# Performance work log

Measured on AMD Instinct MI355X. Metric: run time of the kernel, lower is better.

The kernel has to match this reference:

```python
import jax, jax.numpy as jnp
import numpy as np
import math

N = 20000      # nodes
E = 640000     # edges (avg degree 32)
G = 128        # g_dim (input features)
H1 = 128       # rgcn output dim
H2 = 128       # transformer output dim
R = 8          # num_relations


def setup_inputs() -> dict:
    key = jax.random.key(0)
    ks = jax.random.split(key, 12)
    x = jax.random.normal(ks[0], (N, G), dtype=jnp.float32)
    edge_index = jax.random.randint(ks[1], (2, E), 0, N)
    edge_type = jax.random.randint(ks[2], (E,), 0, R)
    s_in = 1.0 / math.sqrt(G)
    s_h1 = 1.0 / math.sqrt(H1)
    return {
        'x': x,
        'edge_index': edge_index,
        'edge_type': edge_type,
        # RGCNConv params (per-relation weights + root weight + bias)
        'rgcn_weight': jax.random.normal(ks[3], (R, G, H1), dtype=jnp.float32) * s_in,
        'rgcn_root': jax.random.normal(ks[4], (G, H1), dtype=jnp.float32) * s_in,
        'rgcn_bias': jnp.zeros((H1,), dtype=jnp.float32),
        # TransformerConv params (heads=1): query/key/value + skip linear
        'Wq': jax.random.normal(ks[5], (H1, H2), dtype=jnp.float32) * s_h1,
        'bq': jnp.zeros((H2,), dtype=jnp.float32),
        'Wk': jax.random.normal(ks[6], (H1, H2), dtype=jnp.float32) * s_h1,
        'bk': jnp.zeros((H2,), dtype=jnp.float32),
        'Wv': jax.random.normal(ks[7], (H1, H2), dtype=jnp.float32) * s_h1,
        'bv': jnp.zeros((H2,), dtype=jnp.float32),
        'Ws': jax.random.normal(ks[8], (H1, H2), dtype=jnp.float32) * s_h1,
        'bs': jnp.zeros((H2,), dtype=jnp.float32),
    }


def reference(x, edge_index, edge_type, rgcn_weight, rgcn_root, rgcn_bias,
              Wq, bq, Wk, bk, Wv, bv, Ws, bs):
    n = x.shape[0]
    src, dst = edge_index[0], edge_index[1]

    # ---- RGCNConv (aggr='mean' per relation, root weight + bias) ----
    # transform nodes by every relation, then gather per-edge message
    xr = jnp.einsum('ni,rio->nro', x, rgcn_weight)          # [N, R, H1]
    msg = xr[src, edge_type]                                # [E, H1]
    # per (dst, relation) edge counts for mean aggregation
    cnt = jnp.zeros((n, rgcn_weight.shape[0]), x.dtype).at[dst, edge_type].add(1.0)
    denom = jnp.maximum(cnt[dst, edge_type], 1.0)[:, None]  # [E, 1]
    agg = jnp.zeros((n, rgcn_weight.shape[2]), x.dtype).at[dst].add(msg / denom)
    h = agg + x @ rgcn_root + rgcn_bias
    h = jax.nn.relu(h)

    # ---- TransformerConv (heads=1, concat, root_weight=True) ----
    d = Wq.shape[1]
    q = h @ Wq + bq                                          # [N, H2]
    k = h @ Wk + bk
    v = h @ Wv + bv
    score = jnp.sum(q[dst] * k[src], axis=-1) / math.sqrt(d) # [E]
    # softmax over incoming edges of each destination node
    smax = jax.ops.segment_max(score, dst, num_segments=n)   # [N]
    e = jnp.exp(score - smax[dst])                           # [E]
    den = jax.ops.segment_sum(e, dst, num_segments=n)        # [N]
    alpha = e / jnp.maximum(den[dst], 1e-16)                 # [E]
    out = jax.ops.segment_sum(alpha[:, None] * v[src], dst, num_segments=n)
    out = out + h @ Ws + bs                                  # skip connection
    return jax.nn.relu(out)
```

## Files before the change

kernel.cpp:

```cpp
#include <hip/hip_runtime.h>

typedef unsigned short u16;
typedef unsigned int u32;
typedef __attribute__((ext_vector_type(8))) short short8;
typedef __attribute__((ext_vector_type(4))) float f32x4;

#define NN 20000
#define EE 640000
#define SCAN_BLOCKS 80

__device__ inline u16 f2bf(float f) {
    u32 x = __float_as_uint(f);
    return (u16)((x + 0x7FFFu + ((x >> 16) & 1u)) >> 16);
}
__device__ inline float lo16(u32 w) { return __uint_as_float(w << 16); }
__device__ inline float hi16(u32 w) { return __uint_as_float(w & 0xFFFF0000u); }
__device__ inline u32 packbf(float a, float b) { return ((u32)f2bf(b) << 16) | (u32)f2bf(a); }

#define ZP_N (NN * 8)
#define CX_N (NN * 32)
#define WP_N (128 * 1152 + 4 * 128 * 128 + 512)
__global__ __launch_bounds__(256) void prep_all(const float* __restrict__ x,
                                                const float* rw, const float* root,
                                                const float* Wq, const float* Wk,
                                                const float* Wv, const float* Ws,
                                                const float* bq, const float* bk,
                                                const float* bv, const float* bs,
                                                int* __restrict__ cnt, u16* __restrict__ xb,
                                                u16* wt1, u16* wt2, float* bcat) {
    int idx = blockIdx.x * 256 + threadIdx.x;
    if (idx < ZP_N) {
        cnt[idx] = 0;
        return;
    }
    idx -= ZP_N;
    if (idx < CX_N) {
        float4 v = *(const float4*)(x + (size_t)idx * 4);
        uint2 o;
        o.x = packbf(v.x, v.y);
        o.y = packbf(v.z, v.w);
        *(uint2*)(xb + (size_t)idx * 4) = o;
        return;
    }
    idx -= CX_N;
    const int S1 = 128 * 1152, S2 = 4 * 128 * 128;
    if (idx < S1) {
        int o = idx / 1152, k = idx - o * 1152;
        float v = (k < 1024) ? rw[k * 128 + o] : root[(k - 1024) * 128 + o];
        wt1[idx] = f2bf(v);
    } else if (idx < S1 + S2) {
        int j = idx - S1;
        int y = j >> 14, rem = j & 16383, o = rem >> 7, i = rem & 127;
        const float* W = (y == 0) ? Wq : (y == 1) ? Wk : (y == 2) ? Wv : Ws;
        wt2[j] = f2bf(W[i * 128 + o]);
    } else if (idx < S1 + S2 + 512) {
        int j = idx - (S1 + S2);
        int y = j >> 7, c = j & 127;
        const float* b = (y == 0) ? bq : (y == 1) ? bk : (y == 2) ? bv : bs;
        bcat[j] = b[c];
    }
}

__global__ void count_rank(const int* __restrict__ ei, const int* __restrict__ et,
                           int* __restrict__ cnt, int* __restrict__ rank) {
    int base = blockIdx.x * 2048 + threadIdx.x;
#pragma unroll
    for (int j = 0; j < 8; j++) {
        int e = base + j * 256;
        if (e < EE) {
            int dst = ei[EE + e];
            int r = et[e];
            rank[e] = atomicAdd(&cnt[dst * 8 + r], 1);
        }
    }
}

__global__ __launch_bounds__(256) void scan_phase1(const int* __restrict__ cnt,
                                                   int* __restrict__ deg_pref,
                                                   int* __restrict__ blk_sums) {
    __shared__ int lds[256];
    int t = threadIdx.x;
    int n = blockIdx.x * 256 + t;
    int d = 0;
    if (n < NN) {
        int4 c0 = *(const int4*)(cnt + n * 8);
        int4 c1 = *(const int4*)(cnt + n * 8 + 4);
        d = c0.x + c0.y + c0.z + c0.w + c1.x + c1.y + c1.z + c1.w;
    }
    lds[t] = d;
    __syncthreads();
    for (int o = 1; o < 256; o <<= 1) {
        int v = (t >= o) ? lds[t - o] : 0;
        __syncthreads();
        lds[t] += v;
        __syncthreads();
    }
    if (n < NN) deg_pref[n] = lds[t];
    if (t == 255) blk_sums[blockIdx.x] = lds[255];
}

__global__ __launch_bounds__(256) void scan_phase3(const int* __restrict__ cnt,
                                                   const int* __restrict__ deg_pref,
                                                   const int* __restrict__ blk_sums,
                                                   int* __restrict__ row_off,
                                                   int* __restrict__ srt) {
    __shared__ int bs_lds[128];
    int t = threadIdx.x;
    if (t < 128) {
        int v = (t < SCAN_BLOCKS) ? blk_sums[t] : 0;
        bs_lds[t] = v;
    }
    __syncthreads();
    if (t < 128) {
        for (int o = 1; o < 128; o <<= 1) {
            int a = (t >= o) ? bs_lds[t - o] : 0;
            __syncthreads();
            bs_lds[t] += a;
            __syncthreads();
        }
    } else {
        for (int o = 1; o < 128; o <<= 1) {
            __syncthreads();
            __syncthreads();
        }
    }
    int blk_excl = (blockIdx.x > 0) ? bs_lds[blockIdx.x - 1] : 0;
    int n = blockIdx.x * 256 + t;
    if (n >= NN) return;
    int4 c0 = *(const int4*)(cnt + n * 8);
    int4 c1 = *(const int4*)(cnt + n * 8 + 4);
    int deg = c0.x + c0.y + c0.z + c0.w + c1.x + c1.y + c1.z + c1.w;
    int start = blk_excl + deg_pref[n] - deg;
    row_off[n] = start;
    int sub = start;
    int o[8];
    o[0] = sub; sub += c0.x;
    o[1] = sub; sub += c0.y;
    o[2] = sub; sub += c0.z;
    o[3] = sub; sub += c0.w;
    o[4] = sub; sub += c1.x;
    o[5] = sub; sub += c1.y;
    o[6] = sub; sub += c1.z;
    o[7] = sub; sub += c1.w;
    *(int4*)(srt + n * 8) = make_int4(o[0], o[1], o[2], o[3]);
    *(int4*)(srt + n * 8 + 4) = make_int4(o[4], o[5], o[6], o[7]);
    if (n == NN - 1) row_off[NN] = sub;
}

__global__ void scatter_kernel(const int* __restrict__ ei, const int* __restrict__ et,
                               const int* __restrict__ srt, const int* __restrict__ rank,
                               int* __restrict__ es) {
    int base = blockIdx.x * 2048 + threadIdx.x;
#pragma unroll
    for (int j = 0; j < 8; j++) {
        int e = base + j * 256;
        if (e < EE) {
            int dst = ei[EE + e];
            int src = ei[e];
            int r = et[e];
            es[srt[dst * 8 + r] + rank[e]] = src;
        }
    }
}

__global__ __launch_bounds__(256) void rgcn_agg(const u16* __restrict__ xb,
                                                const int* __restrict__ srt,
                                                const int* __restrict__ cnt,
                                                const int* __restrict__ es,
                                                u16* __restrict__ pre) {
    int gid = blockIdx.x * 16 + (threadIdx.x >> 4);
    int lane = threadIdx.x & 15;
    if (gid >= NN * 9) return;
    int node = gid / 9;
    int slot = gid - node * 9;
    long prebase = (long)node * 1152;
    if (slot == 8) {
        uint4 xv = *(const uint4*)(xb + (long)node * 128 + lane * 8);
        *(uint4*)(pre + prebase + 1024 + lane * 8) = xv;
        return;
    }
    int c = cnt[node * 8 + slot];
    int p0 = srt[node * 8 + slot];
    float inv = 1.0f / (float)(c > 1 ? c : 1);
    float a0 = 0.f, a1 = 0.f, a2 = 0.f, a3 = 0.f, a4 = 0.f, a5 = 0.f, a6 = 0.f, a7 = 0.f;
    int i = 0;
    for (; i + 4 <= c; i += 4) {
        int s0 = es[p0 + i], s1 = es[p0 + i + 1], s2 = es[p0 + i + 2], s3 = es[p0 + i + 3];
        uint4 w0 = *(const uint4*)(xb + (long)s0 * 128 + lane * 8);
        uint4 w1 = *(const uint4*)(xb + (long)s1 * 128 + lane * 8);
        uint4 w2 = *(const uint4*)(xb + (long)s2 * 128 + lane * 8);
        uint4 w3 = *(const uint4*)(xb + (long)s3 * 128 + lane * 8);
        a0 += (lo16(w0.x) + lo16(w1.x)) + (lo16(w2.x) + lo16(w3.x));
        a1 += (hi16(w0.x) + hi16(w1.x)) + (hi16(w2.x) + hi16(w3.x));
        a2 += (lo16(w0.y) + lo16(w1.y)) + (lo16(w2.y) + lo16(w3.y));
        a3 += (hi16(w0.y) + hi16(w1.y)) + (hi16(w2.y) + hi16(w3.y));
        a4 += (lo16(w0.z) + lo16(w1.z)) + (lo16(w2.z) + lo16(w3.z));
        a5 += (hi16(w0.z) + hi16(w1.z)) + (hi16(w2.z) + hi16(w3.z));
        a6 += (lo16(w0.w) + lo16(w1.w)) + (lo16(w2.w) + lo16(w3.w));
        a7 += (hi16(w0.w) + hi16(w1.w)) + (hi16(w2.w) + hi16(w3.w));
    }
    for (; i < c; i++) {
        int s = es[p0 + i];
        uint4 w = *(const uint4*)(xb + (long)s * 128 + lane * 8);
        a0 += lo16(w.x); a1 += hi16(w.x); a2 += lo16(w.y); a3 += hi16(w.y);
        a4 += lo16(w.z); a5 += hi16(w.z); a6 += lo16(w.w); a7 += hi16(w.w);
    }
    uint4 ow;
    ow.x = packbf(a0 * inv, a1 * inv);
    ow.y = packbf(a2 * inv, a3 * inv);
    ow.z = packbf(a4 * inv, a5 * inv);
    ow.w = packbf(a6 * inv, a7 * inv);
    *(uint4*)(pre + prebase + slot * 128 + lane * 8) = ow;
}

__global__ __launch_bounds__(256) void gemm_bm32(const u16* __restrict__ A,
                                                 const u16* __restrict__ Bt,
                                                 const float* __restrict__ bias,
                                                 u16* __restrict__ C, int rows) {
    __shared__ u16 As[32 * 136];
    __shared__ u16 Bs[128 * 136];
    int tid = threadIdx.x;
    int w = tid >> 6;
    int lane = tid & 63;
    int quad = lane >> 4;
    int ml = lane & 15;
    int mt = w & 1;
    int nq = w >> 1;
    int block_m = blockIdx.x * 32;

    f32x4 acc[4];
#pragma unroll
    for (int i = 0; i < 4; i++) acc[i] = (f32x4){0.f, 0.f, 0.f, 0.f};

    int rbase = tid >> 4;
    int cb = (tid & 15) * 8;

    for (int kb = 0; kb < 1152; kb += 128) {
#pragma unroll
        for (int rep = 0; rep < 2; rep++) {
            int r = rbase + rep * 16;
            int gr = block_m + r;
            short8 val = {};
            if (gr < rows) val = *(const short8*)(A + (long)gr * 1152 + kb + cb);
            *(short8*)(As + r * 136 + cb) = val;
        }
#pragma unroll
        for (int rep = 0; rep < 8; rep++) {
            int r = rbase + rep * 16;
            short8 val = *(const short8*)(Bt + (long)r * 1152 + kb + cb);
            *(short8*)(Bs + r * 136 + cb) = val;
        }
        __syncthreads();
#pragma unroll
        for (int ks = 0; ks < 4; ks++) {
            short8 af = *(const short8*)(As + (mt * 16 + ml) * 136 + ks * 32 + quad * 8);
#pragma unroll
            for (int nt = 0; nt < 4; nt++) {
                short8 bfr = *(const short8*)(Bs + (nq * 64 + nt * 16 + ml) * 136 + ks * 32 + quad * 8);
                acc[nt] = __builtin_amdgcn_mfma_f32_16x16x32_bf16(af, bfr, acc[nt], 0, 0, 0);
            }
        }
        __syncthreads();
    }
#pragma unroll
    for (int nt = 0; nt < 4; nt++) {
        int col = nq * 64 + nt * 16 + ml;
        float bv = bias[col];
#pragma unroll
        for (int i = 0; i < 4; i++) {
            int gr = block_m + mt * 16 + quad * 4 + i;
            if (gr < rows) {
                float vv = fmaxf(acc[nt][i] + bv, 0.f);
                C[(long)gr * 128 + col] = f2bf(vv);
            }
        }
    }
}

__global__ __launch_bounds__(256) void gemm_qkvs(const u16* __restrict__ A,
                                                 const u16* __restrict__ Bt,
                                                 const float* __restrict__ bias,
                                                 u16* __restrict__ Cq, u16* __restrict__ Ckv,
                                                 u16* __restrict__ Cs, int rows) {
    int y = blockIdx.y;
    Bt += (long)y * 128 * 128;
    bias += y * 128;
    u16* C;
    int ldc;
    if (y == 0) { C = Cq; ldc = 128; }
    else if (y == 1) { C = Ckv; ldc = 256; }
    else if (y == 2) { C = Ckv + 128; ldc = 256; }
    else { C = Cs; ldc = 128; }

    __shared__ u16 As[64 * 136];
    __shared__ u16 Bs[128 * 136];
    int tid = threadIdx.x;
    int w = tid >> 6;
    int lane = tid & 63;
    int quad = lane >> 4;
    int ml = lane & 15;
    int block_m = blockIdx.x * 64;

    f32x4 acc[8];
#pragma unroll
    for (int i = 0; i < 8; i++) acc[i] = (f32x4){0.f, 0.f, 0.f, 0.f};

    int rbase = tid >> 4;
    int cb = (tid & 15) * 8;

#pragma unroll
    for (int rep = 0; rep < 4; rep++) {
        int r = rbase + rep * 16;
        int gr = block_m + r;
        short8 val = {};
        if (gr < rows) val = *(const short8*)(A + (long)gr * 128 + cb);
        *(short8*)(As + r * 136 + cb) = val;
    }
#pragma unroll
    for (int rep = 0; rep < 8; rep++) {
        int r = rbase + rep * 16;
        short8 val = *(const short8*)(Bt + (long)r * 128 + cb);
        *(short8*)(Bs + r * 136 + cb) = val;
    }
    __syncthreads();
#pragma unroll
    for (int ks = 0; ks < 4; ks++) {
        short8 af = *(const short8*)(As + (w * 16 + ml) * 136 + ks * 32 + quad * 8);
#pragma unroll
        for (int nt = 0; nt < 8; nt++) {
            short8 bfr = *(const short8*)(Bs + (nt * 16 + ml) * 136 + ks * 32 + quad * 8);
            acc[nt] = __builtin_amdgcn_mfma_f32_16x16x32_bf16(af, bfr, acc[nt], 0, 0, 0);
        }
    }
#pragma unroll
    for (int nt = 0; nt < 8; nt++) {
        int col = nt * 16 + ml;
        float bv = bias[col];
#pragma unroll
        for (int i = 0; i < 4; i++) {
            int gr = block_m + w * 16 + quad * 4 + i;
            if (gr < rows) {
                C[(long)gr * ldc + col] = f2bf(acc[nt][i] + bv);
            }
        }
    }
}

__global__ __launch_bounds__(256) void attn_kernel(const u16* __restrict__ q,
                                                   const u16* __restrict__ kv,
                                                   const u16* __restrict__ skip,
                                                   const int* __restrict__ row_off,
                                                   const int* __restrict__ es,
                                                   float* __restrict__ out) {
    int node = blockIdx.x * 16 + (threadIdx.x >> 4);
    int lane = threadIdx.x & 15;
    if (node >= NN) return;
    int p0 = row_off[node], p1 = row_off[node + 1];
    uint4 qw = *(const uint4*)(q + (long)node * 128 + lane * 8);
    float q0 = lo16(qw.x), q1 = hi16(qw.x), q2 = lo16(qw.y), q3 = hi16(qw.y);
    float q4 = lo16(qw.z), q5 = hi16(qw.z), q6 = lo16(qw.w), q7 = hi16(qw.w);
    const float SC = 0.08838834764831845f;
    float l = 0.f;
    float a0 = 0.f, a1 = 0.f, a2 = 0.f, a3 = 0.f, a4 = 0.f, a5 = 0.f, a6 = 0.f, a7 = 0.f;
    int p = p0;
    for (; p + 4 <= p1; p += 4) {
        const u16* b0 = kv + (long)es[p] * 256 + lane * 8;
        const u16* b1 = kv + (long)es[p + 1] * 256 + lane * 8;
        const u16* b2 = kv + (long)es[p + 2] * 256 + lane * 8;
        const u16* b3 = kv + (long)es[p + 3] * 256 + lane * 8;
        uint4 k0 = *(const uint4*)b0;
        uint4 k1 = *(const uint4*)b1;
        uint4 k2 = *(const uint4*)b2;
        uint4 k3 = *(const uint4*)b3;
        uint4 v0 = *(const uint4*)(b0 + 128);
        uint4 v1 = *(const uint4*)(b1 + 128);
        uint4 v2 = *(const uint4*)(b2 + 128);
        uint4 v3 = *(const uint4*)(b3 + 128);
        float t0 = q0 * lo16(k0.x) + q1 * hi16(k0.x) + q2 * lo16(k0.y) + q3 * hi16(k0.y) +
                   q4 * lo16(k0.z) + q5 * hi16(k0.z) + q6 * lo16(k0.w) + q7 * hi16(k0.w);
        float t1 = q0 * lo16(k1.x) + q1 * hi16(k1.x) + q2 * lo16(k1.y) + q3 * hi16(k1.y) +
                   q4 * lo16(k1.z) + q5 * hi16(k1.z) + q6 * lo16(k1.w) + q7 * hi16(k1.w);
        float t2 = q0 * lo16(k2.x) + q1 * hi16(k2.x) + q2 * lo16(k2.y) + q3 * hi16(k2.y) +
                   q4 * lo16(k2.z) + q5 * hi16(k2.z) + q6 * lo16(k2.w) + q7 * hi16(k2.w);
        float t3 = q0 * lo16(k3.x) + q1 * hi16(k3.x) + q2 * lo16(k3.y) + q3 * hi16(k3.y) +
                   q4 * lo16(k3.z) + q5 * hi16(k3.z) + q6 * lo16(k3.w) + q7 * hi16(k3.w);
#pragma unroll
        for (int off = 8; off >= 1; off >>= 1) {
            t0 += __shfl_xor(t0, off, 16);
            t1 += __shfl_xor(t1, off, 16);
            t2 += __shfl_xor(t2, off, 16);
            t3 += __shfl_xor(t3, off, 16);
        }
        float w0 = __expf(fminf(t0 * SC, 70.f));
        float w1 = __expf(fminf(t1 * SC, 70.f));
        float w2 = __expf(fminf(t2 * SC, 70.f));
        float w3 = __expf(fminf(t3 * SC, 70.f));
        l += (w0 + w1) + (w2 + w3);
        a0 += w0 * lo16(v0.x) + w1 * lo16(v1.x) + w2 * lo16(v2.x) + w3 * lo16(v3.x);
        a1 += w0 * hi16(v0.x) + w1 * hi16(v1.x) + w2 * hi16(v2.x) + w3 * hi16(v3.x);
        a2 += w0 * lo16(v0.y) + w1 * lo16(v1.y) + w2 * lo16(v2.y) + w3 * lo16(v3.y);
        a3 += w0 * hi16(v0.y) + w1 * hi16(v1.y) + w2 * hi16(v2.y) + w3 * hi16(v3.y);
        a4 += w0 * lo16(v0.z) + w1 * lo16(v1.z) + w2 * lo16(v2.z) + w3 * lo16(v3.z);
        a5 += w0 * hi16(v0.z) + w1 * hi16(v1.z) + w2 * hi16(v2.z) + w3 * hi16(v3.z);
        a6 += w0 * lo16(v0.w) + w1 * lo16(v1.w) + w2 * lo16(v2.w) + w3 * lo16(v3.w);
        a7 += w0 * hi16(v0.w) + w1 * hi16(v1.w) + w2 * hi16(v2.w) + w3 * hi16(v3.w);
    }
    for (; p < p1; p++) {
        const u16* b = kv + (long)es[p] * 256 + lane * 8;
        uint4 kw = *(const uint4*)b;
        uint4 vw = *(const uint4*)(b + 128);
        float t = q0 * lo16(kw.x) + q1 * hi16(kw.x) + q2 * lo16(kw.y) + q3 * hi16(kw.y) +
                  q4 * lo16(kw.z) + q5 * hi16(kw.z) + q6 * lo16(kw.w) + q7 * hi16(kw.w);
#pragma unroll
        for (int off = 8; off >= 1; off >>= 1) t += __shfl_xor(t, off, 16);
        float w = __expf(fminf(t * SC, 70.f));
        l += w;
        a0 += w * lo16(vw.x);
        a1 += w * hi16(vw.x);
        a2 += w * lo16(vw.y);
        a3 += w * hi16(vw.y);
        a4 += w * lo16(vw.z);
        a5 += w * hi16(vw.z);
        a6 += w * lo16(vw.w);
        a7 += w * hi16(vw.w);
    }
    float invl = (l > 0.f) ? 1.0f / l : 0.f;
    uint4 sw = *(const uint4*)(skip + (long)node * 128 + lane * 8);
    float4 oa, ob;
    oa.x = fmaxf(a0 * invl + lo16(sw.x), 0.f);
    oa.y = fmaxf(a1 * invl + hi16(sw.x), 0.f);
    oa.z = fmaxf(a2 * invl + lo16(sw.y), 0.f);
    oa.w = fmaxf(a3 * invl + hi16(sw.y), 0.f);
    ob.x = fmaxf(a4 * invl + lo16(sw.z), 0.f);
    ob.y = fmaxf(a5 * invl + hi16(sw.z), 0.f);
    ob.z = fmaxf(a6 * invl + lo16(sw.w), 0.f);
    ob.w = fmaxf(a7 * invl + hi16(sw.w), 0.f);
    *(float4*)(out + (long)node * 128 + lane * 8) = oa;
    *(float4*)(out + (long)node * 128 + lane * 8 + 4) = ob;
}

extern "C" void kernel_launch(void* const* d_in, const int* in_sizes, int n_in,
                              void* d_out, int out_size, void* d_ws, size_t ws_size,
                              hipStream_t stream) {
    const float* x = (const float*)d_in[0];
    const int* ei = (const int*)d_in[1];
    const int* et = (const int*)d_in[2];
    const float* rw = (const float*)d_in[3];
    const float* root = (const float*)d_in[4];
    const float* rbias = (const float*)d_in[5];
    const float* Wq = (const float*)d_in[6];
    const float* bq = (const float*)d_in[7];
    const float* Wk = (const float*)d_in[8];
    const float* bk = (const float*)d_in[9];
    const float* Wv = (const float*)d_in[10];
    const float* bv = (const float*)d_in[11];
    const float* Ws = (const float*)d_in[12];
    const float* bs = (const float*)d_in[13];

    char* ws = (char*)d_ws;
    size_t off = 0;
    auto alloc = [&](size_t b) {
        size_t o = off;
        off = (off + b + 255) & ~(size_t)255;
        return o;
    };
    u16* pre = (u16*)(ws + alloc((size_t)NN * 1152 * 2));
    u16* h = (u16*)(ws + alloc((size_t)NN * 128 * 2));
    u16* qv = (u16*)(ws + alloc((size_t)NN * 128 * 2));
    u16* kv = (u16*)(ws + alloc((size_t)NN * 256 * 2));
    u16* skip = (u16*)(ws + alloc((size_t)NN * 128 * 2));
    u16* xb = (u16*)(ws + alloc((size_t)NN * 128 * 2));
    u16* wt1 = (u16*)(ws + alloc((size_t)128 * 1152 * 2));
    u16* wt2 = (u16*)(ws + alloc((size_t)4 * 128 * 128 * 2));
    float* bcat = (float*)(ws + alloc((size_t)512 * 4));
    int* cnt = (int*)(ws + alloc((size_t)NN * 8 * 4));
    int* row_off = (int*)(ws + alloc((size_t)(NN + 1) * 4));
    int* srt = (int*)(ws + alloc((size_t)NN * 8 * 4));
    int* deg_pref = (int*)(ws + alloc((size_t)NN * 4));
    int* blk_sums = (int*)(ws + alloc((size_t)128 * 4));
    int* rank = (int*)(ws + alloc((size_t)EE * 4));
    int* es = (int*)(ws + alloc((size_t)EE * 4));
    (void)ws_size;
    (void)in_sizes;
    (void)n_in;
    (void)out_size;

    prep_all<<<(ZP_N + CX_N + WP_N + 255) / 256, 256, 0, stream>>>(
        x, rw, root, Wq, Wk, Wv, Ws, bq, bk, bv, bs, cnt, xb, wt1, wt2, bcat);

    count_rank<<<(EE + 2047) / 2048, 256, 0, stream>>>(ei, et, cnt, rank);
    scan_phase1<<<SCAN_BLOCKS, 256, 0, stream>>>(cnt, deg_pref, blk_sums);
    scan_phase3<<<SCAN_BLOCKS, 256, 0, stream>>>(cnt, deg_pref, blk_sums, row_off, srt);
    scatter_kernel<<<(EE + 2047) / 2048, 256, 0, stream>>>(ei, et, srt, rank, es);

    rgcn_agg<<<(NN * 9 + 15) / 16, 256, 0, stream>>>(xb, srt, cnt, es, pre);

    gemm_bm32<<<(NN + 31) / 32, 256, 0, stream>>>(pre, wt1, rbias, h, NN);
    gemm_qkvs<<<dim3((NN + 63) / 64, 4), 256, 0, stream>>>(h, wt2, bcat, qv, kv, skip, NN);

    attn_kernel<<<(NN + 15) / 16, 256, 0, stream>>>(qv, kv, skip, row_off, es, (float*)d_out);
}
```

Baseline: 247.1 us.

## Fuse RGCN GEMM with QKV/skip projections, keeping h in shared memory

Merges the RGCN output GEMM and the four Q/K/V/skip projection GEMMs into one kernel. Each 32-row block writes the relu'd h tile into shared memory and loops over the four 128x128 weight matrices, so h is never written to or read back from global memory and one launch is dropped. It also removes row bounds checks because NN is a multiple of 32, and halves the attention kernel's block size to 128 threads. The projection weights are now reloaded per 32-row block instead of per 64-row block, and the fused GEMM phase runs serially within each block.

```diff
diff --git a/kernel.cpp b/kernel.cpp
--- a/kernel.cpp
+++ b/kernel.cpp
@@ -213,10 +213,13 @@
     *(uint4*)(pre + prebase + slot * 128 + lane * 8) = ow;
 }
 
-__global__ __launch_bounds__(256) void gemm_bm32(const u16* __restrict__ A,
-                                                 const u16* __restrict__ Bt,
-                                                 const float* __restrict__ bias,
-                                                 u16* __restrict__ C, int rows) {
+__global__ __launch_bounds__(256) void gemm_fused(const u16* __restrict__ A,
+                                                  const u16* __restrict__ Bt1,
+                                                  const float* __restrict__ bias1,
+                                                  const u16* __restrict__ Wt2,
+                                                  const float* __restrict__ bcat,
+                                                  u16* __restrict__ Cq, u16* __restrict__ Ckv,
+                                                  u16* __restrict__ Cs) {
     __shared__ u16 As[32 * 136];
     __shared__ u16 Bs[128 * 136];
     int tid = threadIdx.x;
@@ -239,15 +242,13 @@
 #pragma unroll
         for (int rep = 0; rep < 2; rep++) {
             int r = rbase + rep * 16;
-            int gr = block_m + r;
-            short8 val = {};
-            if (gr < rows) val = *(const short8*)(A + (long)gr * 1152 + kb + cb);
+            short8 val = *(const short8*)(A + (long)(block_m + r) * 1152 + kb + cb);
             *(short8*)(As + r * 136 + cb) = val;
         }
 #pragma unroll
         for (int rep = 0; rep < 8; rep++) {
             int r = rbase + rep * 16;
-            short8 val = *(const short8*)(Bt + (long)r * 1152 + kb + cb);
+            short8 val = *(const short8*)(Bt1 + (long)r * 1152 + kb + cb);
             *(short8*)(Bs + r * 136 + cb) = val;
         }
         __syncthreads();
@@ -265,94 +266,63 @@
 #pragma unroll
     for (int nt = 0; nt < 4; nt++) {
         int col = nq * 64 + nt * 16 + ml;
-        float bv = bias[col];
+        float bv = bias1[col];
 #pragma unroll
         for (int i = 0; i < 4; i++) {
-            int gr = block_m + mt * 16 + quad * 4 + i;
-            if (gr < rows) {
-                float vv = fmaxf(acc[nt][i] + bv, 0.f);
-                C[(long)gr * 128 + col] = f2bf(vv);
+            int r = mt * 16 + quad * 4 + i;
+            As[r * 136 + col] = f2bf(fmaxf(acc[nt][i] + bv, 0.f));
+        }
+    }
+    __syncthreads();
+
+#pragma unroll 1
+    for (int y = 0; y < 4; y++) {
+#pragma unroll
+        for (int rep = 0; rep < 8; rep++) {
+            int r = rbase + rep * 16;
+            short8 val = *(const short8*)(Wt2 + (long)y * 16384 + (long)r * 128 + cb);
+            *(short8*)(Bs + r * 136 + cb) = val;
+        }
+        __syncthreads();
+        f32x4 acc2[4];
+#pragma unroll
+        for (int i = 0; i < 4; i++) acc2[i] = (f32x4){0.f, 0.f, 0.f, 0.f};
+#pragma unroll
+        for (int ks = 0; ks < 4; ks++) {
+            short8 af = *(const short8*)(As + (mt * 16 + ml) * 136 + ks * 32 + quad * 8);
+#pragma unroll
+            for (int nt = 0; nt < 4; nt++) {
+                short8 bfr = *(const short8*)(Bs + (nq * 64 + nt * 16 + ml) * 136 + ks * 32 + quad * 8);
+                acc2[nt] = __builtin_amdgcn_mfma_f32_16x16x32_bf16(af, bfr, acc2[nt], 0, 0, 0);
             }
         }
-    }
-}
-
-__global__ __launch_bounds__(256) void gemm_qkvs(const u16* __restrict__ A,
-                                                 const u16* __restrict__ Bt,
-                                                 const float* __restrict__ bias,
-                                                 u16* __restrict__ Cq, u16* __restrict__ Ckv,
-                                                 u16* __restrict__ Cs, int rows) {
-    int y = blockIdx.y;
-    Bt += (long)y * 128 * 128;
-    bias += y * 128;
-    u16* C;
-    int ldc;
-    if (y == 0) { C = Cq; ldc = 128; }
-    else if (y == 1) { C = Ckv; ldc = 256; }
-    else if (y == 2) { C = Ckv + 128; ldc = 256; }
-    else { C = Cs; ldc = 128; }
-
-    __shared__ u16 As[64 * 136];
-    __shared__ u16 Bs[128 * 136];
-    int tid = threadIdx.x;
-    int w = tid >> 6;
-    int lane = tid & 63;
-    int quad = lane >> 4;
-    int ml = lane & 15;
-    int block_m = blockIdx.x * 64;
-
-    f32x4 acc[8];
-#pragma unroll
-    for (int i = 0; i < 8; i++) acc[i] = (f32x4){0.f, 0.f, 0.f, 0.f};
-
-    int rbase = tid >> 4;
-    int cb = (tid & 15) * 8;
-
-#pragma unroll
-    for (int rep = 0; rep < 4; rep++) {
-        int r = rbase + rep * 16;
-        int gr = block_m + r;
-        short8 val = {};
-        if (gr < rows) val = *(const short8*)(A + (long)gr * 128 + cb);
-        *(short8*)(As + r * 136 + cb) = val;
-    }
-#pragma unroll
-    for (int rep = 0; rep < 8; rep++) {
-        int r = rbase + rep * 16;
-        short8 val = *(const short8*)(Bt + (long)r * 128 + cb);
-        *(short8*)(Bs + r * 136 + cb) = val;
-    }
-    __syncthreads();
-#pragma unroll
-    for (int ks = 0; ks < 4; ks++) {
-        short8 af = *(const short8*)(As + (w * 16 + ml) * 136 + ks * 32 + quad * 8);
-#pragma unroll
-        for (int nt = 0; nt < 8; nt++) {
-            short8 bfr = *(const short8*)(Bs + (nt * 16 + ml) * 136 + ks * 32 + quad * 8);
-            acc[nt] = __builtin_amdgcn_mfma_f32_16x16x32_bf16(af, bfr, acc[nt], 0, 0, 0);
-        }
-    }
-#pragma unroll
-    for (int nt = 0; nt < 8; nt++) {
-        int col = nt * 16 + ml;
-        float bv = bias[col];
-#pragma unroll
-        for (int i = 0; i < 4; i++) {
-            int gr = block_m + w * 16 + quad * 4 + i;
-            if (gr < rows) {
-                C[(long)gr * ldc + col] = f2bf(acc[nt][i] + bv);
+        u16* C;
+        int ldc;
+        if (y == 0) { C = Cq; ldc = 128; }
+        else if (y == 1) { C = Ckv; ldc = 256; }
+        else if (y == 2) { C = Ckv + 128; ldc = 256; }
+        else { C = Cs; ldc = 128; }
+#pragma unroll
+        for (int nt = 0; nt < 4; nt++) {
+            int col = nq * 64 + nt * 16 + ml;
+            float bv = bcat[y * 128 + col];
+#pragma unroll
+            for (int i = 0; i < 4; i++) {
+                int gr = block_m + mt * 16 + quad * 4 + i;
+                C[(long)gr * ldc + col] = f2bf(acc2[nt][i] + bv);
             }
         }
-    }
-}
-
-__global__ __launch_bounds__(256) void attn_kernel(const u16* __restrict__ q,
+        __syncthreads();
+    }
+}
+
+__global__ __launch_bounds__(128) void attn_kernel(const u16* __restrict__ q,
                                                    const u16* __restrict__ kv,
                                                    const u16* __restrict__ skip,
                                                    const int* __restrict__ row_off,
                                                    const int* __restrict__ es,
                                                    float* __restrict__ out) {
-    int node = blockIdx.x * 16 + (threadIdx.x >> 4);
+    int node = blockIdx.x * 8 + (threadIdx.x >> 4);
     int lane = threadIdx.x & 15;
     if (node >= NN) return;
     int p0 = row_off[node], p1 = row_off[node + 1];
@@ -465,7 +435,6 @@
         return o;
     };
     u16* pre = (u16*)(ws + alloc((size_t)NN * 1152 * 2));
-    u16* h = (u16*)(ws + alloc((size_t)NN * 128 * 2));
     u16* qv = (u16*)(ws + alloc((size_t)NN * 128 * 2));
     u16* kv = (u16*)(ws + alloc((size_t)NN * 256 * 2));
     u16* skip = (u16*)(ws + alloc((size_t)NN * 128 * 2));
@@ -495,8 +464,7 @@
 
     rgcn_agg<<<(NN * 9 + 15) / 16, 256, 0, stream>>>(xb, srt, cnt, es, pre);
 
-    gemm_bm32<<<(NN + 31) / 32, 256, 0, stream>>>(pre, wt1, rbias, h, NN);
-    gemm_qkvs<<<dim3((NN + 63) / 64, 4), 256, 0, stream>>>(h, wt2, bcat, qv, kv, skip, NN);
-
-    attn_kernel<<<(NN + 15) / 16, 256, 0, stream>>>(qv, kv, skip, row_off, es, (float*)d_out);
-}
+    gemm_fused<<<NN / 32, 256, 0, stream>>>(pre, wt1, rbias, wt2, bcat, qv, kv, skip);
+
+    attn_kernel<<<(NN + 7) / 8, 128, 0, stream>>>(qv, kv, skip, row_off, es, (float*)d_out);
+}
```

Measured after the change: 235.3 us. 1.05x faster.
